# Optimization experiments

Hardware: AMD Instinct MI355X
Metric: run time of the kernel (lower is better)

## Reference

```python
import jax, jax.numpy as jnp
import numpy as np

B, L, T = 2048, 512, 32


def setup_inputs() -> dict:
    key = jax.random.key(0)
    k1, k2, k3, k4 = jax.random.split(key, 4)
    emit_score = jax.random.normal(k1, (B, L, T), dtype=jnp.float32)
    transition = jax.random.normal(k2, (T, T), dtype=jnp.float32)
    tags = jax.random.randint(k3, (B, L), 0, T, dtype=jnp.int32)
    lengths = jax.random.randint(k4, (B,), 1, L + 1, dtype=jnp.int32)
    return {"emit_score": emit_score, "transition": transition,
            "tags": tags, "lengths": lengths}


def reference(emit_score, transition, tags, lengths):
    # CRF negative log-likelihood (calculate_loss), per-example loss [B].
    b, l, t = emit_score.shape
    mask = jnp.arange(l)[None, :] < lengths[:, None]          # [B,L] bool
    maskf = mask.astype(emit_score.dtype)

    # --- gold path score ---
    gold = jnp.take_along_axis(emit_score, tags[:, :, None], axis=2)[..., 0]  # [B,L]
    trans_gold = transition[tags[:, :-1], tags[:, 1:]]        # [B,L-1]
    gold = gold.at[:, 1:].add(trans_gold)
    total_score = (gold * maskf).sum(axis=1)                  # [B]

    # --- forward algorithm (log partition) via scan over time ---
    emit_tbT = jnp.transpose(emit_score, (1, 0, 2))           # [L,B,T]
    mask_tb = mask.T                                          # [L,B]

    def step(d, x):
        e_t, m_t = x                                          # [B,T], [B]
        # scores[b, prev, next] = d[b,prev] + transition[prev,next] + e_t[b,next]
        scores = d[:, :, None] + transition[None, :, :] + e_t[:, None, :]
        new_d = jax.nn.logsumexp(scores, axis=1)              # [B,T]
        d = jnp.where(m_t[:, None], new_d, d)                 # freeze finished rows
        return d, None

    d0 = emit_tbT[0]                                          # [B,T]
    d, _ = jax.lax.scan(step, d0, (emit_tbT[1:], mask_tb[1:]))
    log_z = jax.nn.logsumexp(d, axis=1)                       # [B]

    return log_z - total_score                                # loss = -llk
```

## Files before the change

### kernel.cpp

```cpp
#include <hip/hip_runtime.h>


constexpr int TT = 32;
constexpr int LL = 512;

#define L2E  1.4426950408889634f
#define LN2f 0.6931471805599453f

template<int X>
__device__ __forceinline__ float swzxf(float v) {
  return __int_as_float(__builtin_amdgcn_ds_swizzle(__float_as_int(v), (X << 10) | 0x1F));
}
__device__ __forceinline__ float rdlf(float v, int k) {
  return __int_as_float(__builtin_amdgcn_readlane(__float_as_int(v), k));
}

template<int DIR>
__device__ __forceinline__ void run_dir(
    const float* __restrict__ erow, const int* __restrict__ trow,
    const float* s_trans, const float (&Eg)[TT],
    int j, int ln, int len, int ns,
    float& a, float& gacc, float& LS)
{
  if (ns <= 0) return;
  const int nf = ns >> 3;
  const int r  = ns & 7;

  float eA[8], eB[8];
  int tvA, tvB;

  auto eload = [&](int s) -> float {
    int t = DIR ? (len - 1 - s) : (1 + s);
    t = t > 0 ? t : 0;
    t = t < LL ? t : LL - 1;
    return erow[t * TT + j];
  };
  auto tload = [&](int s0) -> int {
    int ti = DIR ? (len - 1 - s0 - ln) : (s0 + ln);
    ti = ti > 0 ? ti : 0;
    ti = ti < LL ? ti : LL - 1;
    return trow[ti];
  };
  auto dot = [&](float x) -> float {
    float c0 = 0.f, c1 = 0.f, c2 = 0.f, c3 = 0.f;
#pragma unroll
    for (int q = 0; q < 8; ++q) {
      c0 = fmaf(rdlf(x, 4 * q + 0), Eg[4 * q + 0], c0);
      c1 = fmaf(rdlf(x, 4 * q + 1), Eg[4 * q + 1], c1);
      c2 = fmaf(rdlf(x, 4 * q + 2), Eg[4 * q + 2], c2);
      c3 = fmaf(rdlf(x, 4 * q + 3), Eg[4 * q + 3], c3);
    }
    return (c0 + c1) + (c2 + c3);
  };
  auto renorm = [&]() {
    float mt = fmaxf(a, 1e-30f);
    float m = __int_as_float(__builtin_amdgcn_readfirstlane(__float_as_int(mt)));
    a *= __builtin_amdgcn_rcpf(m);
    LS += __builtin_amdgcn_logf(m);
  };

#define ONESTEP(EC, TVC, K)                                                \
  {                                                                        \
    float F = __builtin_amdgcn_exp2f(EC[K] * L2E);                         \
    int ma = __builtin_amdgcn_readlane(TVC, DIR ? (K) : (K) + 1);          \
    int pv = __builtin_amdgcn_readlane(TVC, DIR ? (K) + 1 : (K));          \
    float tr = s_trans[(pv << 5) + j];                                     \
    if (DIR) a = dot(a * F); else a = dot(a) * F;                          \
    gacc += (j == ma) ? (EC[K] + tr) : 0.f;                                \
  }

#define CHUNK(EC, TVC, EN, TVN, S0)                                        \
  {                                                                        \
    _Pragma("unroll")                                                      \
    for (int k = 0; k < 8; ++k) EN[k] = eload((S0) + 8 + k);               \
    TVN = tload((S0) + 8);                                                 \
    ONESTEP(EC, TVC, 0) ONESTEP(EC, TVC, 1)                                \
    ONESTEP(EC, TVC, 2) ONESTEP(EC, TVC, 3)                                \
    renorm();                                                              \
    ONESTEP(EC, TVC, 4) ONESTEP(EC, TVC, 5)                                \
    ONESTEP(EC, TVC, 6) ONESTEP(EC, TVC, 7)                                \
    renorm();                                                              \
  }

#pragma unroll
  for (int k = 0; k < 8; ++k) eA[k] = eload(k);
  tvA = tload(0);

  int c = 0;
  for (; c + 2 <= nf; c += 2) {
    CHUNK(eA, tvA, eB, tvB, (c + 0) << 3);
    CHUNK(eB, tvB, eA, tvA, (c + 1) << 3);
  }
  if (c < nf) {
    CHUNK(eA, tvA, eB, tvB, c << 3);
    ++c;
  }

#define TAIL(EC, TVC)                                                      \
  {                                                                        \
    if (0 < r) ONESTEP(EC, TVC, 0)                                         \
    if (1 < r) ONESTEP(EC, TVC, 1)                                         \
    if (2 < r) ONESTEP(EC, TVC, 2)                                         \
    if (3 < r) { ONESTEP(EC, TVC, 3) renorm(); }                           \
    if (4 < r) ONESTEP(EC, TVC, 4)                                         \
    if (5 < r) ONESTEP(EC, TVC, 5)                                         \
    if (6 < r) ONESTEP(EC, TVC, 6)                                         \
  }

  if (nf & 1) TAIL(eB, tvB) else TAIL(eA, tvA)

#undef ONESTEP
#undef CHUNK
#undef TAIL
}

__global__ __launch_bounds__(128, 4) void crf_fwd(
    const float* __restrict__ emit, const float* __restrict__ trans,
    const int* __restrict__ tags, const int* __restrict__ lengths,
    float* __restrict__ out, int B)
{
  __shared__ float s_trans[TT * TT];
  __shared__ float s_vec[2][TT];
  __shared__ float s_scl[2][2];
  {
    const float4* t4 = (const float4*)trans;
    float4* st4 = (float4*)s_trans;
    st4[threadIdx.x]       = t4[threadIdx.x];
    st4[threadIdx.x + 128] = t4[threadIdx.x + 128];
  }
  __syncthreads();

  const int j  = threadIdx.x & 31;
  const int ln = threadIdx.x & 63;
  const int wv = threadIdx.x >> 6;
  const int b  = blockIdx.x;

  float Eg[TT];
#pragma unroll
  for (int i = 0; i < TT; ++i) {
    int idx = wv ? (j * TT + i) : (i * TT + j);
    Eg[i] = __builtin_amdgcn_exp2f(s_trans[idx] * L2E);
  }
#pragma unroll
  for (int i = 0; i < TT; ++i) asm volatile("" : "+v"(Eg[i]));

  const int len = lengths[b];
  const int m   = (len - 1) >> 1;
  const int ns  = wv ? (len - 1 - m) : m;
  const float* erow = emit + (size_t)b * (LL * TT);
  const int*   trow = tags + (size_t)b * LL;

  float a, gacc, LS = 0.f;
  if (wv == 0) {
    float e0 = erow[j];
    int   t0 = trow[0];
    a    = __builtin_amdgcn_exp2f(e0 * L2E);
    gacc = (j == t0) ? e0 : 0.f;
  } else {
    a    = 1.f;
    gacc = 0.f;
  }

  if (wv == 0)
    run_dir<0>(erow, trow, s_trans, Eg, j, ln, len, ns, a, gacc, LS);
  else
    run_dir<1>(erow, trow, s_trans, Eg, j, ln, len, ns, a, gacc, LS);

  float gs = gacc;
  gs += swzxf<1>(gs);  gs += swzxf<2>(gs);  gs += swzxf<4>(gs);
  gs += swzxf<8>(gs);  gs += swzxf<16>(gs);

  s_vec[wv][j] = a;
  if (ln == 0) { s_scl[wv][0] = gs; s_scl[wv][1] = LS; }
  __syncthreads();

  if (wv == 0) {
    float p = s_vec[0][j] * s_vec[1][j];
    p += swzxf<1>(p);  p += swzxf<2>(p);  p += swzxf<4>(p);
    p += swzxf<8>(p);  p += swzxf<16>(p);
    float logz = (__builtin_amdgcn_logf(p) + s_scl[0][1] + s_scl[1][1]) * LN2f;
    if (threadIdx.x == 0) out[b] = logz - (s_scl[0][0] + s_scl[1][0]);
  }
}

extern "C" void kernel_launch(void* const* d_in, const int* in_sizes, int n_in,
                              void* d_out, int out_size, void* d_ws, size_t ws_size,
                              hipStream_t stream) {
  const float* emit    = (const float*)d_in[0];
  const float* trans   = (const float*)d_in[1];
  const int*   tags    = (const int*)d_in[2];
  const int*   lengths = (const int*)d_in[3];
  float*       out     = (float*)d_out;
  const int B = in_sizes[3];
  hipLaunchKernelGGL(crf_fwd, dim3(B), dim3(128), 0, stream,
                     emit, trans, tags, lengths, out, B);
}
```

Measured before the change: 278.6 us.

## Unify forward/backward CRF recursions using transposed transition table in shared memory

Stores both the transition matrix and its transpose in shared memory so each wavefront can run the same forward-style recurrence (dot then multiply by exp(emit)) in its own direction. The backward wave now starts from the last emission, and the middle transition is added explicitly at the end. Gold-score lookups are batched per chunk of eight steps with readlanes hoisted ahead of the dependent chain. The tail loop becomes a simple runtime loop. This adds 4 KB of shared memory and changes the split arithmetic, which risks edge-case bugs for short lengths.

```diff
diff --git a/kernel.cpp b/kernel.cpp
--- a/kernel.cpp
+++ b/kernel.cpp
@@ -14,33 +14,63 @@
 __device__ __forceinline__ float rdlf(float v, int k) {
   return __int_as_float(__builtin_amdgcn_readlane(__float_as_int(v), k));
 }
+__device__ __forceinline__ int rdli(int v, int k) {
+  return __builtin_amdgcn_readlane(v, k);
+}
 
-template<int DIR>
-__device__ __forceinline__ void run_dir(
-    const float* __restrict__ erow, const int* __restrict__ trow,
-    const float* s_trans, const float (&Eg)[TT],
-    int j, int ln, int len, int ns,
-    float& a, float& gacc, float& LS)
+__global__ __launch_bounds__(128, 4) void crf_fwd(
+    const float* __restrict__ emit, const float* __restrict__ trans,
+    const int* __restrict__ tags, const int* __restrict__ lengths,
+    float* __restrict__ out, int B)
 {
-  if (ns <= 0) return;
-  const int nf = ns >> 3;
-  const int r  = ns & 7;
+  __shared__ float s_tr[2][TT * TT];
+  __shared__ float s_vec[2][TT];
+  __shared__ float s_scl[2][2];
 
-  float eA[8], eB[8];
-  int tvA, tvB;
+  {
+#pragma unroll
+    for (int k = 0; k < 8; ++k) {
+      int idx = threadIdx.x + 128 * k;
+      float v = trans[idx];
+      int rI = idx >> 5, cI = idx & 31;
+      s_tr[0][idx] = v;
+      s_tr[1][(cI << 5) | rI] = v;
+    }
+  }
+  __syncthreads();
 
-  auto eload = [&](int s) -> float {
-    int t = DIR ? (len - 1 - s) : (1 + s);
-    t = t > 0 ? t : 0;
-    t = t < LL ? t : LL - 1;
-    return erow[t * TT + j];
-  };
-  auto tload = [&](int s0) -> int {
-    int ti = DIR ? (len - 1 - s0 - ln) : (s0 + ln);
-    ti = ti > 0 ? ti : 0;
-    ti = ti < LL ? ti : LL - 1;
-    return trow[ti];
-  };
+  const int j  = threadIdx.x & 31;
+  const int ln = threadIdx.x & 63;
+  const int wv = threadIdx.x >> 6;
+  const int b  = blockIdx.x;
+
+  const float* tb = s_tr[wv];
+
+  float Eg[TT];
+#pragma unroll
+  for (int i = 0; i < TT; ++i)
+    Eg[i] = __builtin_amdgcn_exp2f(tb[i * TT + j] * L2E);
+#pragma unroll
+  for (int i = 0; i < TT; ++i) asm volatile("" : "+v"(Eg[i]));
+
+  const int len = lengths[b];
+  const int m   = (len - 1) >> 1;
+  const float* erow = emit + (size_t)b * (LL * TT);
+  const int*   trow = tags + (size_t)b * LL;
+
+  int ns, dt, tinit;
+  if (wv == 0) { ns = m;                      dt =  1; tinit = 0;       }
+  else         { ns = len - 2 - m; if (ns < 0) ns = 0; dt = -1; tinit = len - 1; }
+
+  float a, gacc, LS = 0.f;
+  if (wv == 1 && len < 2) { a = 1.f; gacc = 0.f; }
+  else {
+    float e0 = erow[tinit * TT + j];
+    int   t0 = trow[tinit];
+    a    = __builtin_amdgcn_exp2f(e0 * L2E);
+    gacc = (j == t0) ? e0 : 0.f;
+  }
+
   auto dot = [&](float x) -> float {
     float c0 = 0.f, c1 = 0.f, c2 = 0.f, c3 = 0.f;
 #pragma unroll
@@ -54,117 +84,74 @@
   };
   auto renorm = [&]() {
     float mt = fmaxf(a, 1e-30f);
-    float m = __int_as_float(__builtin_amdgcn_readfirstlane(__float_as_int(mt)));
-    a *= __builtin_amdgcn_rcpf(m);
-    LS += __builtin_amdgcn_logf(m);
+    float mm = __int_as_float(__builtin_amdgcn_readfirstlane(__float_as_int(mt)));
+    a *= __builtin_amdgcn_rcpf(mm);
+    LS += __builtin_amdgcn_logf(mm);
   };
+  auto clampi = [](int t) -> int { t = t > 0 ? t : 0; return t < LL ? t : LL - 1; };
 
-#define ONESTEP(EC, TVC, K)                                                \
-  {                                                                        \
-    float F = __builtin_amdgcn_exp2f(EC[K] * L2E);                         \
-    int ma = __builtin_amdgcn_readlane(TVC, DIR ? (K) : (K) + 1);          \
-    int pv = __builtin_amdgcn_readlane(TVC, DIR ? (K) + 1 : (K));          \
-    float tr = s_trans[(pv << 5) + j];                                     \
-    if (DIR) a = dot(a * F); else a = dot(a) * F;                          \
-    gacc += (j == ma) ? (EC[K] + tr) : 0.f;                                \
+  const int nf = ns >> 3;
+  const int rr = ns & 7;
+
+  float Ab[8], Bb[8];
+  int tvA, tvB;
+#pragma unroll
+  for (int k = 0; k < 8; ++k) Ab[k] = erow[clampi(tinit + dt * (1 + k)) * TT + j];
+  tvA = trow[clampi(tinit + dt * ln)];
+
+  for (int c = 0; c < nf; ++c) {
+    const int s0n = (c + 1) << 3;
+#pragma unroll
+    for (int k = 0; k < 8; ++k)
+      Bb[k] = erow[clampi(tinit + dt * (1 + s0n + k)) * TT + j];
+    tvB = trow[clampi(tinit + dt * (s0n + ln))];
+
+    int g0 = rdli(tvA, 0), g1 = rdli(tvA, 1), g2 = rdli(tvA, 2), g3 = rdli(tvA, 3),
+        g4 = rdli(tvA, 4), g5 = rdli(tvA, 5), g6 = rdli(tvA, 6), g7 = rdli(tvA, 7),
+        g8 = rdli(tvA, 8);
+    float t0v = tb[(g0 << 5) + j], t1v = tb[(g1 << 5) + j];
+    float t2v = tb[(g2 << 5) + j], t3v = tb[(g3 << 5) + j];
+    float t4v = tb[(g4 << 5) + j], t5v = tb[(g5 << 5) + j];
+    float t6v = tb[(g6 << 5) + j], t7v = tb[(g7 << 5) + j];
+    float F0 = __builtin_amdgcn_exp2f(Ab[0] * L2E);
+    float F1 = __builtin_amdgcn_exp2f(Ab[1] * L2E);
+    float F2 = __builtin_amdgcn_exp2f(Ab[2] * L2E);
+    float F3 = __builtin_amdgcn_exp2f(Ab[3] * L2E);
+    float F4 = __builtin_amdgcn_exp2f(Ab[4] * L2E);
+    float F5 = __builtin_amdgcn_exp2f(Ab[5] * L2E);
+    float F6 = __builtin_amdgcn_exp2f(Ab[6] * L2E);
+    float F7 = __builtin_amdgcn_exp2f(Ab[7] * L2E);
+
+    a = dot(a) * F0;  gacc += (j == g1) ? (Ab[0] + t0v) : 0.f;
+    a = dot(a) * F1;  gacc += (j == g2) ? (Ab[1] + t1v) : 0.f;
+    a = dot(a) * F2;  gacc += (j == g3) ? (Ab[2] + t2v) : 0.f;
+    a = dot(a) * F3;  gacc += (j == g4) ? (Ab[3] + t3v) : 0.f;
+    renorm();
+    a = dot(a) * F4;  gacc += (j == g5) ? (Ab[4] + t4v) : 0.f;
+    a = dot(a) * F5;  gacc += (j == g6) ? (Ab[5] + t5v) : 0.f;
+    a = dot(a) * F6;  gacc += (j == g7) ? (Ab[6] + t6v) : 0.f;
+    a = dot(a) * F7;  gacc += (j == g8) ? (Ab[7] + t7v) : 0.f;
+    renorm();
+
+#pragma unroll
+    for (int k = 0; k < 8; ++k) Ab[k] = Bb[k];
+    tvA = tvB;
   }
 
-#define CHUNK(EC, TVC, EN, TVN, S0)                                        \
-  {                                                                        \
-    _Pragma("unroll")                                                      \
-    for (int k = 0; k < 8; ++k) EN[k] = eload((S0) + 8 + k);               \
-    TVN = tload((S0) + 8);                                                 \
-    ONESTEP(EC, TVC, 0) ONESTEP(EC, TVC, 1)                                \
-    ONESTEP(EC, TVC, 2) ONESTEP(EC, TVC, 3)                                \
-    renorm();                                                              \
-    ONESTEP(EC, TVC, 4) ONESTEP(EC, TVC, 5)                                \
-    ONESTEP(EC, TVC, 6) ONESTEP(EC, TVC, 7)                                \
-    renorm();                                                              \
+  for (int k = 0; k < rr; ++k) {
+    int s = (nf << 3) + k;
+    int t = tinit + dt * (1 + s);
+    float e  = erow[t * TT + j];
+    int  ga  = trow[t - dt];
+    int  gb  = trow[t];
+    float tr = tb[(ga << 5) + j];
+    float F  = __builtin_amdgcn_exp2f(e * L2E);
+    a = dot(a) * F;
+    gacc += (j == gb) ? (e + tr) : 0.f;
+    if ((k & 3) == 3) renorm();
   }
 
-#pragma unroll
-  for (int k = 0; k < 8; ++k) eA[k] = eload(k);
-  tvA = tload(0);
-
-  int c = 0;
-  for (; c + 2 <= nf; c += 2) {
-    CHUNK(eA, tvA, eB, tvB, (c + 0) << 3);
-    CHUNK(eB, tvB, eA, tvA, (c + 1) << 3);
-  }
-  if (c < nf) {
-    CHUNK(eA, tvA, eB, tvB, c << 3);
-    ++c;
-  }
-
-#define TAIL(EC, TVC)                                                      \
-  {                                                                        \
-    if (0 < r) ONESTEP(EC, TVC, 0)                                         \
-    if (1 < r) ONESTEP(EC, TVC, 1)                                         \
-    if (2 < r) ONESTEP(EC, TVC, 2)                                         \
-    if (3 < r) { ONESTEP(EC, TVC, 3) renorm(); }                           \
-    if (4 < r) ONESTEP(EC, TVC, 4)                                         \
-    if (5 < r) ONESTEP(EC, TVC, 5)                                         \
-    if (6 < r) ONESTEP(EC, TVC, 6)                                         \
-  }
-
-  if (nf & 1) TAIL(eB, tvB) else TAIL(eA, tvA)
-
-#undef ONESTEP
-#undef CHUNK
-#undef TAIL
-}
-
-__global__ __launch_bounds__(128, 4) void crf_fwd(
-    const float* __restrict__ emit, const float* __restrict__ trans,
-    const int* __restrict__ tags, const int* __restrict__ lengths,
-    float* __restrict__ out, int B)
-{
-  __shared__ float s_trans[TT * TT];
-  __shared__ float s_vec[2][TT];
-  __shared__ float s_scl[2][2];
-  {
-    const float4* t4 = (const float4*)trans;
-    float4* st4 = (float4*)s_trans;
-    st4[threadIdx.x]       = t4[threadIdx.x];
-    st4[threadIdx.x + 128] = t4[threadIdx.x + 128];
-  }
-  __syncthreads();
-
-  const int j  = threadIdx.x & 31;
-  const int ln = threadIdx.x & 63;
-  const int wv = threadIdx.x >> 6;
-  const int b  = blockIdx.x;
-
-  float Eg[TT];
-#pragma unroll
-  for (int i = 0; i < TT; ++i) {
-    int idx = wv ? (j * TT + i) : (i * TT + j);
-    Eg[i] = __builtin_amdgcn_exp2f(s_trans[idx] * L2E);
-  }
-#pragma unroll
-  for (int i = 0; i < TT; ++i) asm volatile("" : "+v"(Eg[i]));
-
-  const int len = lengths[b];
-  const int m   = (len - 1) >> 1;
-  const int ns  = wv ? (len - 1 - m) : m;
-  const float* erow = emit + (size_t)b * (LL * TT);
-  const int*   trow = tags + (size_t)b * LL;
-
-  float a, gacc, LS = 0.f;
-  if (wv == 0) {
-    float e0 = erow[j];
-    int   t0 = trow[0];
-    a    = __builtin_amdgcn_exp2f(e0 * L2E);
-    gacc = (j == t0) ? e0 : 0.f;
-  } else {
-    a    = 1.f;
-    gacc = 0.f;
-  }
-
-  if (wv == 0)
-    run_dir<0>(erow, trow, s_trans, Eg, j, ln, len, ns, a, gacc, LS);
-  else
-    run_dir<1>(erow, trow, s_trans, Eg, j, ln, len, ns, a, gacc, LS);
+  if (wv == 0 && len >= 2) a = dot(a);
 
   float gs = gacc;
   gs += swzxf<1>(gs);  gs += swzxf<2>(gs);  gs += swzxf<4>(gs);
@@ -179,7 +166,14 @@
     p += swzxf<1>(p);  p += swzxf<2>(p);  p += swzxf<4>(p);
     p += swzxf<8>(p);  p += swzxf<16>(p);
     float logz = (__builtin_amdgcn_logf(p) + s_scl[0][1] + s_scl[1][1]) * LN2f;
-    if (threadIdx.x == 0) out[b] = logz - (s_scl[0][0] + s_scl[1][0]);
+    if (threadIdx.x == 0) {
+      float gm = 0.f;
+      if (len >= 2) {
+        int tm = trow[m], tn = trow[m + 1];
+        gm = s_tr[0][(tm << 5) + tn];
+      }
+      out[b] = logz - (s_scl[0][0] + s_scl[1][0] + gm);
+    }
   }
 }
 
```

New measurement: 282.8 us. No clear change (+1.5%).
